# Kernel optimization log

Hardware: AMD Instinct MI355X
Metric: run time of the kernel (lower is better)

Reference implementation:

```python
import jax, jax.numpy as jnp
import numpy as np

HID = 2048
HEADS = 16
HD = HID // HEADS  # 128
EPS = 1e-6


def setup_inputs() -> dict:
    key = jax.random.key(0)
    ks = jax.random.split(key, 9)
    s = 1.0 / np.sqrt(HID)
    return {
        "hidden_states": jax.random.normal(ks[0], (4, 4096, HID), jnp.float32),
        "q_w": jax.random.normal(ks[1], (HID, HID), jnp.float32) * s,
        "q_b": jnp.zeros((HID,), jnp.float32),
        "k_w": jax.random.normal(ks[2], (HID, HID), jnp.float32) * s,
        "k_b": jnp.zeros((HID,), jnp.float32),
        "v_w": jax.random.normal(ks[3], (HID, HID), jnp.float32) * s,
        "v_b": jnp.zeros((HID,), jnp.float32),
        "o_w": jax.random.normal(ks[4], (HID, HID), jnp.float32) * s,
        "o_b": jnp.zeros((HID,), jnp.float32),
    }


def _heads(x, b, s):
    # [B,S,HID] -> [B,H,S,Dh]
    return x.reshape(b, s, HEADS, HD).transpose(0, 2, 1, 3)


def reference(hidden_states, q_w, q_b, k_w, k_b, v_w, v_b, o_w, o_b):
    b, s, _ = hidden_states.shape
    # torch Linear: y = x @ W.T + b
    q = _heads(hidden_states @ q_w.T + q_b, b, s)
    k = _heads(hidden_states @ k_w.T + k_b, b, s)
    v = _heads(hidden_states @ v_w.T + v_b, b, s)
    # kernel feature map: elu(x) + 1
    qp = jax.nn.elu(q) + 1.0
    kp = jax.nn.elu(k) + 1.0
    # KV outer-product reduction over sequence: [B,H,Dh,Dh]
    kv = jnp.einsum('bhsd,bhse->bhde', kp, v)
    # normalizer z = q' @ sum_s k'  -> [B,H,S,1]
    z = jnp.einsum('bhsd,bhd->bhs', qp, kp.sum(axis=2))[..., None]
    attn = jnp.einsum('bhsd,bhde->bhse', qp, kv) / (z + EPS)
    out = attn.transpose(0, 2, 1, 3).reshape(b, s, HID)
    return out @ o_w.T + o_b
```

## Files before the change

### kernel.cpp

```cpp
#include <hip/hip_runtime.h>
#include <hip/hip_bf16.h>

#define HIDC 2048
#define NHEADS 16
#define HDIM 128
#define NB 4
#define NS 4096
#define NROWS (NB*NS)
#define QSTR 6144
#define EPSV 1e-6f

typedef __attribute__((ext_vector_type(8))) short s16x8;
typedef __attribute__((ext_vector_type(4))) float f32x4;
typedef __attribute__((ext_vector_type(8))) unsigned short u16x8;

static __device__ __forceinline__ unsigned short f2b(float f) {
  unsigned int u = __float_as_uint(f);
  u += 0x7fffu + ((u >> 16) & 1u);
  return (unsigned short)(u >> 16);
}
static __device__ __forceinline__ float b2f(unsigned short h) {
  return __uint_as_float(((unsigned int)h) << 16);
}

static __device__ __forceinline__ void gload_lds16(const unsigned short* g, unsigned short* l) {
  __builtin_amdgcn_global_load_lds(
      (const __attribute__((address_space(1))) void*)g,
      (__attribute__((address_space(3))) void*)l, 16, 0, 0);
}

__global__ __launch_bounds__(256) void convert_all(
    const float* __restrict__ hs, const float* __restrict__ qw,
    const float* __restrict__ kw, const float* __restrict__ vw,
    const float* __restrict__ ow,
    unsigned short* __restrict__ hsb, unsigned short* __restrict__ qwb,
    unsigned short* __restrict__ kwb, unsigned short* __restrict__ vwb,
    unsigned short* __restrict__ owb)
{
  int bid = blockIdx.x;
  const float* src; unsigned short* dst; size_t base;
  if (bid < 16384) { src = hs; dst = hsb; base = (size_t)bid << 11; }
  else {
    int t = bid - 16384; int wsel = t >> 11; int wb = t & 2047;
    src = wsel == 0 ? qw : wsel == 1 ? kw : wsel == 2 ? vw : ow;
    dst = wsel == 0 ? qwb : wsel == 1 ? kwb : wsel == 2 ? vwb : owb;
    base = (size_t)wb << 11;
  }
  size_t i = base + ((size_t)threadIdx.x << 3);
  float4 a = *(const float4*)(src + i);
  float4 b = *(const float4*)(src + i + 4);
  u16x8 o;
  o[0] = f2b(a.x); o[1] = f2b(a.y); o[2] = f2b(a.z); o[3] = f2b(a.w);
  o[4] = f2b(b.x); o[5] = f2b(b.y); o[6] = f2b(b.z); o[7] = f2b(b.w);
  *(u16x8*)(dst + i) = o;
}

template<int QKV, int OUT_BF16>
__global__ __launch_bounds__(512, 2) void gemm256(
    const unsigned short* __restrict__ A,
    const unsigned short* __restrict__ B0,
    const unsigned short* __restrict__ B1,
    const unsigned short* __restrict__ B2,
    const float* __restrict__ bias0,
    const float* __restrict__ bias1,
    const float* __restrict__ bias2,
    void* __restrict__ Cp,
    int ntile, int astr, int ostr)
{
  __shared__ unsigned short lds[65536];
  const int tid = threadIdx.x;
  const int lane = tid & 63, wid = tid >> 6;
  const int wr = wid >> 2, wc = wid & 3;
  const int l15 = lane & 15, l4 = lane >> 4;

  const int cpx = (int)gridDim.x >> 3;
  const int bidx = (int)blockIdx.x;
  const int wg = (bidx & 7) * cpx + (bidx >> 3);
  const int csz = ntile << 2;
  const int chunk = wg / csz;
  const int t = wg % csz;
  const int bm = ((chunk << 2) + (t & 3)) << 8;
  const int bn = (t >> 2) << 8;

  const unsigned short* Bp = B0;
  const float* bias = bias0;
  bool act = false;
  int bnw = bn;
  if (QKV) {
    int seg = bn >> 11;
    Bp = seg == 0 ? B0 : (seg == 1 ? B1 : B2);
    bias = seg == 0 ? bias0 : (seg == 1 ? bias1 : bias2);
    act = seg < 2;
    bnw = bn & 2047;
  }

  const int c0 = wid << 1;
  const int srow = lane >> 2;
  const int scol = (((lane & 3) ^ ((srow >> 1) & 3)) << 3);
  const unsigned short* Asrc0 = A + (size_t)(bm + (c0 << 4) + srow) * astr + scol;
  const unsigned short* Asrc1 = Asrc0 + (size_t)16 * astr;
  const unsigned short* Bsrc0 = Bp + (size_t)(bnw + (c0 << 4) + srow) * HIDC + scol;
  const unsigned short* Bsrc1 = Bsrc0 + (size_t)16 * HIDC;
  const int adst = c0 << 9;

  const int xa = ((l4 ^ ((l15 >> 1) & 3)) << 3);
  const int abase = ((wr << 7) + l15) * 32 + xa;
  const int bbase = 8192 + ((wc << 6) + l15) * 32 + xa;

  f32x4 acc[8][4] = {};

#define STAGE_A(s_) { const int sl_ = ((s_) & 3) << 14; const int kt_ = (s_) << 5; \
    gload_lds16(Asrc0 + kt_, &lds[sl_ + adst]); \
    gload_lds16(Asrc1 + kt_, &lds[sl_ + adst + 512]); }
#define STAGE_B(s_) { const int sl_ = ((s_) & 3) << 14; const int kt_ = (s_) << 5; \
    gload_lds16(Bsrc0 + kt_, &lds[sl_ + 8192 + adst]); \
    gload_lds16(Bsrc1 + kt_, &lds[sl_ + 8192 + adst + 512]); }

#define MM4(ai_, r_) { \
    acc[r_][0] = __builtin_amdgcn_mfma_f32_16x16x32_bf16(ai_, b0, acc[r_][0], 0, 0, 0); \
    acc[r_][1] = __builtin_amdgcn_mfma_f32_16x16x32_bf16(ai_, b1, acc[r_][1], 0, 0, 0); \
    acc[r_][2] = __builtin_amdgcn_mfma_f32_16x16x32_bf16(ai_, b2, acc[r_][2], 0, 0, 0); \
    acc[r_][3] = __builtin_amdgcn_mfma_f32_16x16x32_bf16(ai_, b3, acc[r_][3], 0, 0, 0); }

#define DO_STEP(s_, STG, GATE) { \
    const int sl = ((s_) & 3) << 14; \
     \
    s16x8 b0 = *(const s16x8*)&lds[sl + bbase]; \
    s16x8 b1 = *(const s16x8*)&lds[sl + bbase + 512]; \
    s16x8 b2 = *(const s16x8*)&lds[sl + bbase + 1024]; \
    s16x8 b3 = *(const s16x8*)&lds[sl + bbase + 1536]; \
    s16x8 a0 = *(const s16x8*)&lds[sl + abase]; \
    s16x8 a1 = *(const s16x8*)&lds[sl + abase + 512]; \
    s16x8 a2 = *(const s16x8*)&lds[sl + abase + 1024]; \
    s16x8 a3 = *(const s16x8*)&lds[sl + abase + 1536]; \
    if (STG) STAGE_A((s_) + 3); \
    __builtin_amdgcn_s_barrier(); \
    asm volatile("s_waitcnt lgkmcnt(0)" ::: "memory"); \
    __builtin_amdgcn_s_setprio(1); \
    MM4(a0, 0) MM4(a1, 1) MM4(a2, 2) MM4(a3, 3) \
    __builtin_amdgcn_s_setprio(0); \
    __builtin_amdgcn_s_barrier(); \
     \
    s16x8 a4 = *(const s16x8*)&lds[sl + abase + 2048]; \
    s16x8 a5 = *(const s16x8*)&lds[sl + abase + 2560]; \
    s16x8 a6 = *(const s16x8*)&lds[sl + abase + 3072]; \
    s16x8 a7 = *(const s16x8*)&lds[sl + abase + 3584]; \
    if (STG) STAGE_B((s_) + 3); \
    __builtin_amdgcn_s_barrier(); \
    asm volatile("s_waitcnt lgkmcnt(0)" ::: "memory"); \
    __builtin_amdgcn_s_setprio(1); \
    MM4(a4, 4) MM4(a5, 5) MM4(a6, 6) MM4(a7, 7) \
    __builtin_amdgcn_s_setprio(0); \
    if ((GATE) == 8)      { asm volatile("s_waitcnt vmcnt(8)" ::: "memory"); } \
    else if ((GATE) == 4) { asm volatile("s_waitcnt vmcnt(4)" ::: "memory"); } \
    else if ((GATE) == 0) { asm volatile("s_waitcnt vmcnt(0)" ::: "memory"); } \
    __builtin_amdgcn_s_barrier(); \
  }

  STAGE_A(0); STAGE_B(0);
  STAGE_A(1); STAGE_B(1);
  STAGE_A(2); STAGE_B(2);
  asm volatile("s_waitcnt vmcnt(8)" ::: "memory");
  __builtin_amdgcn_s_barrier();

  for (int s = 0; s < 61; ++s) DO_STEP(s, 1, 8);
  DO_STEP(61, 0, 4);
  DO_STEP(62, 0, 0);
  DO_STEP(63, 0, -1);

#undef DO_STEP
#undef MM4
#undef STAGE_A
#undef STAGE_B

  #pragma unroll
  for (int nf = 0; nf < 4; ++nf) {
    const int colw = (wc << 6) + (nf << 4) + l15;
    const float bv = bias[bnw + colw];
    #pragma unroll
    for (int mf = 0; mf < 8; ++mf) {
      #pragma unroll
      for (int r = 0; r < 4; ++r) {
        const int row = bm + (wr << 7) + (mf << 4) + (l4 << 2) + r;
        float v = acc[mf][nf][r] + bv;
        if (QKV) { if (act) v = (v > 0.f) ? (v + 1.f) : __expf(v); }
        const size_t off = (size_t)row * ostr + bn + colw;
        if (OUT_BF16) ((unsigned short*)Cp)[off] = f2b(v);
        else          ((float*)Cp)[off] = v;
      }
    }
  }
}

__global__ __launch_bounds__(256) void kv_partial(
    const unsigned short* __restrict__ kp, const unsigned short* __restrict__ vv,
    float* __restrict__ kvp, float* __restrict__ ksp)
{
  const int bh = blockIdx.x >> 3;
  const int chunk = blockIdx.x & 7;
  const int b = bh >> 4, h = bh & 15;
  const int tid = threadIdx.x;
  const int td = tid >> 4, te = tid & 15;

  __shared__ float kpl[32][128];
  __shared__ float vl[32][132];

  float acc[8][8] = {};
  float ks[8] = {};

  const size_t rowbase = (size_t)b * NS * QSTR + (size_t)h * HDIM;
  const int s0 = chunk * 512;

  for (int st = 0; st < 512; st += 32) {
    __syncthreads();
    #pragma unroll
    for (int i = 0; i < 2; ++i) {
      int idx = tid + (i << 8);
      int row = idx >> 4, q = idx & 15;
      size_t g = rowbase + (size_t)(s0 + st + row) * QSTR + (q << 3);
      u16x8 k8 = *(const u16x8*)(kp + g);
      u16x8 v8 = *(const u16x8*)(vv + g);
      float tk[8], tv[8];
      #pragma unroll
      for (int j = 0; j < 8; ++j) { tk[j] = b2f(k8[j]); tv[j] = b2f(v8[j]); }
      *(float4*)&kpl[row][(q << 3)]     = make_float4(tk[0], tk[1], tk[2], tk[3]);
      *(float4*)&kpl[row][(q << 3) + 4] = make_float4(tk[4], tk[5], tk[6], tk[7]);
      *(float4*)&vl[row][(q << 3)]      = make_float4(tv[0], tv[1], tv[2], tv[3]);
      *(float4*)&vl[row][(q << 3) + 4]  = make_float4(tv[4], tv[5], tv[6], tv[7]);
    }
    __syncthreads();
    #pragma unroll 4
    for (int s = 0; s < 32; ++s) {
      float kd[8], ve[8];
      *(float4*)&kd[0] = *(const float4*)&kpl[s][td << 3];
      *(float4*)&kd[4] = *(const float4*)&kpl[s][(td << 3) + 4];
      *(float4*)&ve[0] = *(const float4*)&vl[s][te << 3];
      *(float4*)&ve[4] = *(const float4*)&vl[s][(te << 3) + 4];
      if (te == 0) {
        #pragma unroll
        for (int i = 0; i < 8; ++i) ks[i] += kd[i];
      }
      #pragma unroll
      for (int i = 0; i < 8; ++i)
        #pragma unroll
        for (int j = 0; j < 8; ++j)
          acc[i][j] += kd[i] * ve[j];
    }
  }

  float* outp = kvp + ((size_t)(chunk * 64 + bh) << 14);
  #pragma unroll
  for (int j = 0; j < 8; ++j) {
    int e = (te << 3) + j;
    float r0[8];
    #pragma unroll
    for (int i = 0; i < 8; ++i) r0[i] = acc[i][j];
    *(float4*)&outp[(size_t)e * HDIM + (td << 3)]     = *(float4*)&r0[0];
    *(float4*)&outp[(size_t)e * HDIM + (td << 3) + 4] = *(float4*)&r0[4];
  }
  if (te == 0) {
    float* kso = ksp + ((size_t)(chunk * 64 + bh) << 7) + (td << 3);
    #pragma unroll
    for (int i = 0; i < 8; ++i) kso[i] = ks[i];
  }
}

__global__ __launch_bounds__(256) void kv_reduce(
    const float* __restrict__ kvp, float* __restrict__ kvT)
{
  int i = blockIdx.x * 256 + threadIdx.x;
  float s = 0.f;
  #pragma unroll
  for (int c = 0; c < 8; ++c) s += kvp[(size_t)c * (64 * 16384) + i];
  kvT[i] = s;
}

__global__ __launch_bounds__(256) void attn_ker(
    const unsigned short* __restrict__ qp, const float* __restrict__ kvT,
    const float* __restrict__ ksp, unsigned short* __restrict__ attn)
{
  const int bh = blockIdx.x >> 5, stile = blockIdx.x & 31;
  const int b = bh >> 4, h = bh & 15;
  const int tid = threadIdx.x;
  const int lane = tid & 63, w = tid >> 6;
  const int l15 = lane & 15, l4 = lane >> 4;

  __shared__ unsigned short Qs[128][136];
  __shared__ unsigned short Ks[128][136];
  __shared__ float ksl[128];
  __shared__ float zs[128];

  const size_t qbase = ((size_t)b * NS + (size_t)stile * 128) * QSTR + (size_t)h * HDIM;

  #pragma unroll
  for (int i = 0; i < 8; ++i) {
    int idx = tid + (i << 8);
    int row = idx >> 4, q = idx & 15;
    u16x8 v8 = *(const u16x8*)(qp + qbase + (size_t)row * QSTR + (q << 3));
    *(u16x8*)&Qs[row][q << 3] = v8;
  }
  const float* kvb = kvT + ((size_t)bh << 14);
  #pragma unroll
  for (int i = 0; i < 16; ++i) {
    int idx = tid + (i << 8);
    int row = idx >> 5, q = idx & 31;
    float4 v4 = *(const float4*)(kvb + (size_t)row * HDIM + (q << 2));
    ushort4 w4; w4.x = f2b(v4.x); w4.y = f2b(v4.y); w4.z = f2b(v4.z); w4.w = f2b(v4.w);
    *(ushort4*)&Ks[row][q << 2] = w4;
  }
  if (tid < 128) {
    float s = 0.f;
    #pragma unroll
    for (int c = 0; c < 8; ++c) s += ksp[((size_t)(c * 64 + bh) << 7) + tid];
    ksl[tid] = s;
  }
  __syncthreads();
  if (tid < 128) {
    float z = 0.f;
    #pragma unroll
    for (int dq = 0; dq < 16; ++dq) {
      u16x8 qv = *(const u16x8*)&Qs[tid][dq << 3];
      #pragma unroll
      for (int j = 0; j < 8; ++j) z += b2f(qv[j]) * ksl[(dq << 3) + j];
    }
    zs[tid] = 1.f / (z + EPSV);
  }
  __syncthreads();

  f32x4 acc[2][8] = {};
  #pragma unroll
  for (int kk = 0; kk < 4; ++kk) {
    s16x8 a[2], bb[8];
    #pragma unroll
    for (int mf = 0; mf < 2; ++mf)
      a[mf] = *(const s16x8*)&Qs[(w << 5) + (mf << 4) + l15][(kk << 5) + (l4 << 3)];
    #pragma unroll
    for (int nf = 0; nf < 8; ++nf)
      bb[nf] = *(const s16x8*)&Ks[(nf << 4) + l15][(kk << 5) + (l4 << 3)];
    #pragma unroll
    for (int mf = 0; mf < 2; ++mf)
      #pragma unroll
      for (int nf = 0; nf < 8; ++nf)
        acc[mf][nf] = __builtin_amdgcn_mfma_f32_16x16x32_bf16(a[mf], bb[nf], acc[mf][nf], 0, 0, 0);
  }

  #pragma unroll
  for (int mf = 0; mf < 2; ++mf) {
    #pragma unroll
    for (int r = 0; r < 4; ++r) {
      const int rl = (w << 5) + (mf << 4) + (l4 << 2) + r;
      const float zi = zs[rl];
      #pragma unroll
      for (int nf = 0; nf < 8; ++nf) {
        const int e = (nf << 4) + l15;
        attn[qbase + (size_t)rl * QSTR + e] = f2b(acc[mf][nf][r] * zi);
      }
    }
  }
}

extern "C" void kernel_launch(void* const* d_in, const int* in_sizes, int n_in,
                              void* d_out, int out_size, void* d_ws, size_t ws_size,
                              hipStream_t stream) {
  const float* hs = (const float*)d_in[0];
  const float* qw = (const float*)d_in[1];
  const float* qb = (const float*)d_in[2];
  const float* kw = (const float*)d_in[3];
  const float* kb = (const float*)d_in[4];
  const float* vw = (const float*)d_in[5];
  const float* vb = (const float*)d_in[6];
  const float* ow = (const float*)d_in[7];
  const float* ob = (const float*)d_in[8];

  char* w = (char*)d_ws;
  unsigned short* hsb = (unsigned short*)(w);
  unsigned short* qwb = (unsigned short*)(w + 67108864);
  unsigned short* kwb = (unsigned short*)(w + 75497472);
  unsigned short* vwb = (unsigned short*)(w + 83886080);
  unsigned short* owb = (unsigned short*)(w + 92274688);
  unsigned short* qkv = (unsigned short*)(w + 100663296);
  float* kvp = (float*)(w);
  float* ksp = (float*)(w + 33554432);
  float* kvT = (float*)(w + 33816576);

  convert_all<<<dim3(24576), dim3(256), 0, stream>>>(hs, qw, kw, vw, ow, hsb, qwb, kwb, vwb, owb);
  gemm256<1, 1><<<dim3(24 * 64), dim3(512), 0, stream>>>(
      hsb, qwb, kwb, vwb, qb, kb, vb, qkv, 24, HIDC, QSTR);
  kv_partial<<<dim3(512), dim3(256), 0, stream>>>(qkv + 2048, qkv + 4096, kvp, ksp);
  kv_reduce<<<dim3(4096), dim3(256), 0, stream>>>(kvp, kvT);
  attn_ker<<<dim3(2048), dim3(256), 0, stream>>>(qkv, kvT, ksp, qkv + 4096);
  gemm256<0, 0><<<dim3(8 * 64), dim3(512), 0, stream>>>(
      qkv + 4096, owb, owb, owb, ob, ob, ob, d_out, 8, QSTR, HIDC);
}
```

Measured before the change: 783.8 us.

## Prefetch next-stage LDS fragments into double-buffered registers in GEMM mainloop

Restructures the GEMM K-loop so the B and low-A fragments for the next K step are read from LDS into a second register set while the current step's MFMAs run. The upper-A fragments are loaded at the start of each step. The explicit lgkmcnt(0) waits are removed, and the vmcnt gate moves to the middle of the step so the next buffer is resident before it is read. The goal is to hide LDS read latency behind MFMA work, at the cost of more VGPRs and a more delicate ordering of the barrier and wait sequence.

```diff
diff --git a/kernel.cpp b/kernel.cpp
--- a/kernel.cpp
+++ b/kernel.cpp
@@ -108,6 +108,9 @@
   const int bbase = 8192 + ((wc << 6) + l15) * 32 + xa;
 
   f32x4 acc[8][4] = {};
+  s16x8 bfr[2][4];
+  s16x8 alo[2][4];
+  s16x8 ahi[4];
 
 #define STAGE_A(s_) { const int sl_ = ((s_) & 3) << 14; const int kt_ = (s_) << 5; \
     gload_lds16(Asrc0 + kt_, &lds[sl_ + adst]); \
@@ -116,44 +119,49 @@
     gload_lds16(Bsrc0 + kt_, &lds[sl_ + 8192 + adst]); \
     gload_lds16(Bsrc1 + kt_, &lds[sl_ + 8192 + adst + 512]); }
 
-#define MM4(ai_, r_) { \
-    acc[r_][0] = __builtin_amdgcn_mfma_f32_16x16x32_bf16(ai_, b0, acc[r_][0], 0, 0, 0); \
-    acc[r_][1] = __builtin_amdgcn_mfma_f32_16x16x32_bf16(ai_, b1, acc[r_][1], 0, 0, 0); \
-    acc[r_][2] = __builtin_amdgcn_mfma_f32_16x16x32_bf16(ai_, b2, acc[r_][2], 0, 0, 0); \
-    acc[r_][3] = __builtin_amdgcn_mfma_f32_16x16x32_bf16(ai_, b3, acc[r_][3], 0, 0, 0); }
-
-#define DO_STEP(s_, STG, GATE) { \
+#define MM4(ai_, r_, P_) { \
+    acc[r_][0] = __builtin_amdgcn_mfma_f32_16x16x32_bf16(ai_, bfr[P_][0], acc[r_][0], 0, 0, 0); \
+    acc[r_][1] = __builtin_amdgcn_mfma_f32_16x16x32_bf16(ai_, bfr[P_][1], acc[r_][1], 0, 0, 0); \
+    acc[r_][2] = __builtin_amdgcn_mfma_f32_16x16x32_bf16(ai_, bfr[P_][2], acc[r_][2], 0, 0, 0); \
+    acc[r_][3] = __builtin_amdgcn_mfma_f32_16x16x32_bf16(ai_, bfr[P_][3], acc[r_][3], 0, 0, 0); }
+
+#define DO_STEP(s_, P_, STG, GATE, NEXT) { \
     const int sl = ((s_) & 3) << 14; \
      \
-    s16x8 b0 = *(const s16x8*)&lds[sl + bbase]; \
-    s16x8 b1 = *(const s16x8*)&lds[sl + bbase + 512]; \
-    s16x8 b2 = *(const s16x8*)&lds[sl + bbase + 1024]; \
-    s16x8 b3 = *(const s16x8*)&lds[sl + bbase + 1536]; \
-    s16x8 a0 = *(const s16x8*)&lds[sl + abase]; \
-    s16x8 a1 = *(const s16x8*)&lds[sl + abase + 512]; \
-    s16x8 a2 = *(const s16x8*)&lds[sl + abase + 1024]; \
-    s16x8 a3 = *(const s16x8*)&lds[sl + abase + 1536]; \
+    ahi[0] = *(const s16x8*)&lds[sl + abase + 2048]; \
+    ahi[1] = *(const s16x8*)&lds[sl + abase + 2560]; \
+    ahi[2] = *(const s16x8*)&lds[sl + abase + 3072]; \
+    ahi[3] = *(const s16x8*)&lds[sl + abase + 3584]; \
     if (STG) STAGE_A((s_) + 3); \
+    __builtin_amdgcn_sched_barrier(0); \
     __builtin_amdgcn_s_barrier(); \
-    asm volatile("s_waitcnt lgkmcnt(0)" ::: "memory"); \
     __builtin_amdgcn_s_setprio(1); \
-    MM4(a0, 0) MM4(a1, 1) MM4(a2, 2) MM4(a3, 3) \
+    MM4(alo[P_][0], 0, P_) MM4(alo[P_][1], 1, P_) \
+    MM4(alo[P_][2], 2, P_) MM4(alo[P_][3], 3, P_) \
     __builtin_amdgcn_s_setprio(0); \
+    if ((GATE) == 6)      { asm volatile("s_waitcnt vmcnt(6)" ::: "memory"); } \
+    else if ((GATE) == 4) { asm volatile("s_waitcnt vmcnt(4)" ::: "memory"); } \
+    else if ((GATE) == 0) { asm volatile("s_waitcnt vmcnt(0)" ::: "memory"); } \
     __builtin_amdgcn_s_barrier(); \
      \
-    s16x8 a4 = *(const s16x8*)&lds[sl + abase + 2048]; \
-    s16x8 a5 = *(const s16x8*)&lds[sl + abase + 2560]; \
-    s16x8 a6 = *(const s16x8*)&lds[sl + abase + 3072]; \
-    s16x8 a7 = *(const s16x8*)&lds[sl + abase + 3584]; \
+    if (NEXT) { \
+      const int sln = (((s_) + 1) & 3) << 14; \
+      bfr[1-(P_)][0] = *(const s16x8*)&lds[sln + bbase]; \
+      bfr[1-(P_)][1] = *(const s16x8*)&lds[sln + bbase + 512]; \
+      bfr[1-(P_)][2] = *(const s16x8*)&lds[sln + bbase + 1024]; \
+      bfr[1-(P_)][3] = *(const s16x8*)&lds[sln + bbase + 1536]; \
+      alo[1-(P_)][0] = *(const s16x8*)&lds[sln + abase]; \
+      alo[1-(P_)][1] = *(const s16x8*)&lds[sln + abase + 512]; \
+      alo[1-(P_)][2] = *(const s16x8*)&lds[sln + abase + 1024]; \
+      alo[1-(P_)][3] = *(const s16x8*)&lds[sln + abase + 1536]; \
+    } \
     if (STG) STAGE_B((s_) + 3); \
+    __builtin_amdgcn_sched_barrier(0); \
     __builtin_amdgcn_s_barrier(); \
-    asm volatile("s_waitcnt lgkmcnt(0)" ::: "memory"); \
     __builtin_amdgcn_s_setprio(1); \
-    MM4(a4, 4) MM4(a5, 5) MM4(a6, 6) MM4(a7, 7) \
+    MM4(ahi[0], 4, P_) MM4(ahi[1], 5, P_) \
+    MM4(ahi[2], 6, P_) MM4(ahi[3], 7, P_) \
     __builtin_amdgcn_s_setprio(0); \
-    if ((GATE) == 8)      { asm volatile("s_waitcnt vmcnt(8)" ::: "memory"); } \
-    else if ((GATE) == 4) { asm volatile("s_waitcnt vmcnt(4)" ::: "memory"); } \
-    else if ((GATE) == 0) { asm volatile("s_waitcnt vmcnt(0)" ::: "memory"); } \
     __builtin_amdgcn_s_barrier(); \
   }
 
@@ -162,11 +170,23 @@
   STAGE_A(2); STAGE_B(2);
   asm volatile("s_waitcnt vmcnt(8)" ::: "memory");
   __builtin_amdgcn_s_barrier();
-
-  for (int s = 0; s < 61; ++s) DO_STEP(s, 1, 8);
-  DO_STEP(61, 0, 4);
-  DO_STEP(62, 0, 0);
-  DO_STEP(63, 0, -1);
+  bfr[0][0] = *(const s16x8*)&lds[bbase];
+  bfr[0][1] = *(const s16x8*)&lds[bbase + 512];
+  bfr[0][2] = *(const s16x8*)&lds[bbase + 1024];
+  bfr[0][3] = *(const s16x8*)&lds[bbase + 1536];
+  alo[0][0] = *(const s16x8*)&lds[abase];
+  alo[0][1] = *(const s16x8*)&lds[abase + 512];
+  alo[0][2] = *(const s16x8*)&lds[abase + 1024];
+  alo[0][3] = *(const s16x8*)&lds[abase + 1536];
+
+  for (int s = 0; s < 60; s += 2) {
+    DO_STEP(s,     0, 1, 6, 1)
+    DO_STEP(s + 1, 1, 1, 6, 1)
+  }
+  DO_STEP(60, 0, 1, 6, 1)
+  DO_STEP(61, 1, 0, 4, 1)
+  DO_STEP(62, 0, 0, 0, 1)
+  DO_STEP(63, 1, 0, -1, 0)
 
 #undef DO_STEP
 #undef MM4
```

Result: no change. 774.4 us (-1.2%).
